# Optimization experiments

Measured on AMD Instinct MI355X. Metric: run time of the kernel, lower is better.

## Reference

```python
import jax, jax.numpy as jnp
import numpy as np

B, S, D, H = 2, 2048, 1024, 16
HD = D // H  # head_dim = 64
ROPE_BASE = 10000.0


def _rope_tables(seq_len, head_dim, dtype):
    inv_freq = 1.0 / (ROPE_BASE ** (jnp.arange(0, head_dim, 2, dtype=jnp.float32) / head_dim))
    t = jnp.arange(seq_len, dtype=jnp.float32)
    freqs = jnp.outer(t, inv_freq)                      # [S, HD/2]
    emb = jnp.concatenate([freqs, freqs], axis=-1)      # [S, HD]
    return jnp.cos(emb).astype(dtype), jnp.sin(emb).astype(dtype)


def _rotate_half(x):
    x1, x2 = jnp.split(x, 2, axis=-1)
    return jnp.concatenate([-x2, x1], axis=-1)


def setup_inputs() -> dict:
    key = jax.random.key(0)
    k0, k1, k2, k3, k4 = jax.random.split(key, 5)
    std = 0.02
    return {
        "hidden_states": jax.random.normal(k0, (B, S, D), dtype=jnp.float32),
        "attention_mask": jnp.ones((B, S), dtype=jnp.int32),
        "Wq": jax.random.normal(k1, (D, D), dtype=jnp.float32) * std,
        "Wk": jax.random.normal(k2, (D, D), dtype=jnp.float32) * std,
        "Wv": jax.random.normal(k3, (D, D), dtype=jnp.float32) * std,
        "Wo": jax.random.normal(k4, (D, D), dtype=jnp.float32) * std,
    }


def reference(hidden_states, attention_mask, Wq, Wk, Wv, Wo):
    b, s, d = hidden_states.shape
    scale = HD ** -0.5

    # torch Linear (no bias): y = x @ W.T, then split heads -> [b, h, s, hd]
    def proj_heads(W):
        y = jnp.einsum('bsd,ed->bse', hidden_states, W)
        return y.reshape(b, s, H, HD).transpose(0, 2, 1, 3)

    q, k, v = proj_heads(Wq), proj_heads(Wk), proj_heads(Wv)

    cos, sin = _rope_tables(s, HD, q.dtype)   # [s, hd]
    cos, sin = cos[None, None], sin[None, None]
    q = q * cos + _rotate_half(q) * sin
    k = k * cos + _rotate_half(k) * sin

    attn = jnp.einsum('bhqd,bhkd->bhqk', q, k) * scale  # [b,h,s,s]
    # mask [b,s] broadcast over heads and query dim (matches expand in torch)
    attn = jnp.where(attention_mask[:, None, None, :] == 0, -jnp.inf, attn)
    attn = jax.nn.softmax(attn, axis=-1)

    out = jnp.einsum('bhqk,bhkd->bhqd', attn, v)
    out = out.transpose(0, 2, 1, 3).reshape(b, s, d)
    return jnp.einsum('bsd,ed->bse', out, Wo)
```

## Files before the change

kernel.cpp:

```cpp
#include <hip/hip_runtime.h>
#include <math.h>

#define B_  2
#define S_  2048
#define D_  1024
#define H_  16
#define HD_ 64
#define M_  (B_*S_)

typedef __attribute__((ext_vector_type(8)))  short s8v;
typedef __attribute__((ext_vector_type(4)))  int   i4v;
typedef __attribute__((ext_vector_type(4)))  float f4v;
typedef __attribute__((ext_vector_type(16))) float f16x;
#define MFMA16(a,b,c) __builtin_amdgcn_mfma_f32_16x16x32_bf16(a,b,c,0,0,0)
#define MFMA32(a,b,c) __builtin_amdgcn_mfma_f32_32x32x16_bf16(a,b,c,0,0,0)

typedef __attribute__((address_space(1))) const unsigned int uint_ga;
typedef __attribute__((address_space(3))) unsigned int       uint_ls;

__device__ __forceinline__ unsigned short f2bf(float x) {
    unsigned u = __float_as_uint(x);
    u += 0x7FFF + ((u >> 16) & 1);
    return (unsigned short)(u >> 16);
}
__device__ __forceinline__ void gld16(const unsigned short* g, short* l) {
    __builtin_amdgcn_global_load_lds((uint_ga*)g, (uint_ls*)l, 16, 0, 0);
}

#define SCALE2 0.1803368801111204f
#define MXF2   16.0f

__global__ __launch_bounds__(256) void cvt_bf16_kernel(
    const float* __restrict__ X,  const float* __restrict__ Wq,
    const float* __restrict__ Wk, const float* __restrict__ Wv,
    const float* __restrict__ Wo,
    unsigned short* __restrict__ Xb,  unsigned short* __restrict__ Wqb,
    unsigned short* __restrict__ Wkb, unsigned short* __restrict__ Wvb,
    unsigned short* __restrict__ Wob, float2* __restrict__ cst)
{
    int y = blockIdx.y;
    if (y == 5) {
        int i = blockIdx.x * 256 + threadIdx.x;
        if (i < S_ * 32) {
            int j = i >> 11, s = i & 2047;
            double inv = pow(10000.0, -(double)j / 32.0);
            double ang = (double)s * inv;
            cst[i] = make_float2((float)cos(ang), (float)sin(ang));
        }
        return;
    }
    const float* src = (y==0)?X:(y==1)?Wq:(y==2)?Wk:(y==3)?Wv:Wo;
    unsigned short* dst = (y==0)?Xb:(y==1)?Wqb:(y==2)?Wkb:(y==3)?Wvb:Wob;
    int n = (y==0) ? (M_*D_) : (D_*D_);
    int i = (blockIdx.x*256 + threadIdx.x)*4;
    if (i >= n) return;
    float4 v = *(const float4*)&src[i];
    ushort4 o;
    o.x = f2bf(v.x); o.y = f2bf(v.y); o.z = f2bf(v.z); o.w = f2bf(v.w);
    *(ushort4*)&dst[i] = o;
}

__device__ __forceinline__ void mfma_128x128(
    const unsigned short* __restrict__ Amat, const unsigned short* __restrict__ Bmat,
    int m0, int n0, short* As, short* Bs, f4v acc[4][4])
{
    int tid = threadIdx.x;
    int l = tid & 63, w = tid >> 6;
    int wm = w >> 1, wn = w & 1;
    int lm = l & 15, qd = l >> 4;
    int lm7 = lm & 7;

    f4v z = {0.f, 0.f, 0.f, 0.f};
#pragma unroll
    for (int mt = 0; mt < 4; mt++)
#pragma unroll
        for (int nt = 0; nt < 4; nt++) acc[mt][nt] = z;

    int rl = l >> 3;
    int kc = (l & 7) ^ rl;
    const unsigned short* aG = Amat + (size_t)(m0 + w*32 + rl) * D_ + kc*8;
    const unsigned short* bG = Bmat + (size_t)(n0 + w*32 + rl) * D_ + kc*8;
    short* aL = As + (w*32)*64;
    short* bL = Bs + (w*32)*64;

#pragma unroll 1
    for (int k0 = 0; k0 < D_; k0 += 64) {
        __syncthreads();
#pragma unroll
        for (int j = 0; j < 4; j++) {
            gld16(aG + k0 + (size_t)j*8*D_, aL + j*8*64);
            gld16(bG + k0 + (size_t)j*8*D_, bL + j*8*64);
        }
        __syncthreads();
#pragma unroll
        for (int half = 0; half < 2; half++) {
            int pc = (half*4 + qd) ^ lm7;
            s8v afr[4], bfr[4];
#pragma unroll
            for (int x = 0; x < 4; x++) {
                afr[x] = *(const s8v*)(As + ((wm*64 + x*16 + lm)*8 + pc)*8);
                bfr[x] = *(const s8v*)(Bs + ((wn*64 + x*16 + lm)*8 + pc)*8);
            }
#pragma unroll
            for (int mt = 0; mt < 4; mt++)
#pragma unroll
                for (int nt = 0; nt < 4; nt++)
                    acc[mt][nt] = MFMA16(afr[mt], bfr[nt], acc[mt][nt]);
        }
    }
}

__global__ __launch_bounds__(256, 2) void qkv_mfma_kernel(
    const unsigned short* __restrict__ Xb,
    const unsigned short* __restrict__ Wqb, const unsigned short* __restrict__ Wkb,
    const unsigned short* __restrict__ Wvb, const float2* __restrict__ cst,
    unsigned short* __restrict__ Q, unsigned short* __restrict__ K,
    unsigned short* __restrict__ Vt)
{
    __shared__ __align__(16) short As[8192], Bs[8192];
    int bx = blockIdx.x, by = blockIdx.y;
    int proj = by >> 3, f8 = by & 7;
    int l = threadIdx.x & 63, w = threadIdx.x >> 6;
    int wm = w >> 1, wn = w & 1, lm = l & 15, qd = l >> 4;

    f4v acc[4][4];
    if (proj < 2) {
        const unsigned short* Wm = proj ? Wkb : Wqb;
        mfma_128x128(Wm, Xb, f8*128, bx*128, As, Bs, acc);

        int b  = (bx*128) >> 11;
        int sb = ((bx*128) & 2047) + wn*64;
        int bh = b*H_ + f8*2 + wm;
        unsigned short* dst = proj ? K : Q;
        float post = proj ? 1.0f : SCALE2;
#pragma unroll
        for (int mt = 0; mt < 4; mt++) {
            float sgn = (mt < 2) ? -1.f : 1.f;
#pragma unroll
            for (int nt = 0; nt < 4; nt++) {
                int s = sb + nt*16 + lm;
                unsigned short ov[4];
#pragma unroll
                for (int r = 0; r < 4; r++) {
                    int d = mt*16 + qd*4 + r;
                    float2 cs = cst[(d & 31)*S_ + s];
                    float v = acc[mt][nt][r];
                    float p = acc[mt^2][nt][r];
                    ov[r] = f2bf((v*cs.x + sgn*p*cs.y) * post);
                }
                ushort4 ou; ou.x=ov[0]; ou.y=ov[1]; ou.z=ov[2]; ou.w=ov[3];
                *(ushort4*)&dst[((size_t)bh*S_ + s)*HD_ + mt*16 + qd*4] = ou;
            }
        }
    } else {
        mfma_128x128(Xb, Wvb, bx*128, f8*128, As, Bs, acc);

        int b  = (bx*128) >> 11;
        int sb = ((bx*128) & 2047) + wm*64;
        int bh = b*H_ + f8*2 + wn;
#pragma unroll
        for (int mt = 0; mt < 4; mt++)
#pragma unroll
            for (int nt = 0; nt < 4; nt++) {
                int dim = nt*16 + lm;
                int s   = sb + mt*16 + qd*4;
                ushort4 ou;
                ou.x = f2bf(acc[mt][nt][0]);
                ou.y = f2bf(acc[mt][nt][1]);
                ou.z = f2bf(acc[mt][nt][2]);
                ou.w = f2bf(acc[mt][nt][3]);
                *(ushort4*)&Vt[((size_t)bh*HD_ + dim)*S_ + s] = ou;
            }
    }
}

__global__ __launch_bounds__(256, 2) void flash_mfma_kernel(
    const unsigned short* __restrict__ Q, const unsigned short* __restrict__ K,
    const unsigned short* __restrict__ Vt, const int* __restrict__ mask,
    unsigned short* __restrict__ AO)
{
    __shared__ __align__(16) short Ksh[2][4096];
    __shared__ __align__(16) short Vsh[2][4096];
    __shared__ __align__(16) float msk[S_];

    int bh = blockIdx.y;
    int b = bh >> 4, h = bh & 15;
    int tid = threadIdx.x;
    int l = tid & 63, w = tid >> 6;
    int lq = l & 31, hf = l >> 5;
    int q0 = blockIdx.x * 128 + w * 32;

    {
        int i0 = tid * 8;
        const int* mp = mask + b * S_ + i0;
#pragma unroll
        for (int jj = 0; jj < 8; jj++)
            msk[i0 + jj] = mp[jj] ? -MXF2 : -3.0e38f;
    }

    const unsigned short* Qr = Q + ((size_t)bh * S_ + q0 + lq) * HD_ + hf * 8;
    s8v qf[4];
#pragma unroll
    for (int dc = 0; dc < 4; dc++) qf[dc] = *(const s8v*)(Qr + dc * 16);

    f16x zz = {0.f};
    f16x oacc[2]; oacc[0] = zz; oacc[1] = zz;
    f16x lacc = zz;
    s8v ones;
#pragma unroll
    for (int j = 0; j < 8; j++) ones[j] = (short)0x3F80;

    const unsigned short* Kb = K  + (size_t)bh * S_ * HD_;
    const unsigned short* Vb = Vt + (size_t)bh * HD_ * S_;

    int fb0 = 2*w, fb1 = 2*w + 1;
    const unsigned short* kS0 = Kb + (size_t)((fb0>>2)*32 + lq) * HD_ + (fb0&3)*16 + hf*8;
    const unsigned short* kS1 = Kb + (size_t)((fb1>>2)*32 + lq) * HD_ + (fb1&3)*16 + hf*8;
    const unsigned short* vS0 = Vb + (size_t)((fb0>>2)*32 + lq) * S_  + (fb0&3)*16 + hf*8;
    const unsigned short* vS1 = Vb + (size_t)((fb1>>2)*32 + lq) * S_  + (fb1&3)*16 + hf*8;

    s8v kr0 = *(const s8v*)(kS0);
    s8v kr1 = *(const s8v*)(kS1);
    s8v vr0 = *(const s8v*)(vS0);
    s8v vr1 = *(const s8v*)(vS1);

#pragma unroll 1
    for (int t = 0; t < S_ / 64; t++) {
        int buf = t & 1;
        *(s8v*)(&Ksh[buf][fb0*512 + l*8]) = kr0;
        *(s8v*)(&Ksh[buf][fb1*512 + l*8]) = kr1;
        *(s8v*)(&Vsh[buf][fb0*512 + l*8]) = vr0;
        *(s8v*)(&Vsh[buf][fb1*512 + l*8]) = vr1;
        __syncthreads();
        if (t < S_/64 - 1) {
            int koff = (t + 1) * 64;
            kr0 = *(const s8v*)(kS0 + (size_t)koff * HD_);
            kr1 = *(const s8v*)(kS1 + (size_t)koff * HD_);
            vr0 = *(const s8v*)(vS0 + koff);
            vr1 = *(const s8v*)(vS1 + koff);
        }

        int mb = t * 64;
        f16x sa0, sa1;
#pragma unroll
        for (int g = 0; g < 4; g++) {
            f4v m0 = *(const f4v*)&msk[mb + g*8 + hf*4];
            f4v m1 = *(const f4v*)&msk[mb + 32 + g*8 + hf*4];
#pragma unroll
            for (int i = 0; i < 4; i++) { sa0[g*4+i] = m0[i]; sa1[g*4+i] = m1[i]; }
        }
#pragma unroll
        for (int dc = 0; dc < 4; dc++) {
            s8v kf0 = *(const s8v*)(&Ksh[buf][(0*4+dc)*512 + l*8]);
            sa0 = MFMA32(kf0, qf[dc], sa0);
        }
#pragma unroll
        for (int dc = 0; dc < 4; dc++) {
            s8v kf1 = *(const s8v*)(&Ksh[buf][(1*4+dc)*512 + l*8]);
            sa1 = MFMA32(kf1, qf[dc], sa1);
        }

        float p[32];
#pragma unroll
        for (int r = 0; r < 16; r++) p[r]      = exp2f(sa0[r]);
#pragma unroll
        for (int r = 0; r < 16; r++) p[16 + r] = exp2f(sa1[r]);

        int pk[16];
#pragma unroll
        for (int m = 0; m < 16; m++)
            pk[m] = __builtin_amdgcn_perm(__float_as_uint(p[2*m+1]),
                                          __float_as_uint(p[2*m]), 0x07060302);

#pragma unroll
        for (int kcc = 0; kcc < 4; kcc++) {
            int a = 4*kcc;
            int x01 = hf ? pk[a]   : pk[a+2];
            int x23 = hf ? pk[a+1] : pk[a+3];
            int y01 = __shfl_xor(x01, 32);
            int y23 = __shfl_xor(x23, 32);
            i4v fr;
            fr.x = hf ? y01 : pk[a];
            fr.y = hf ? y23 : pk[a+1];
            fr.z = hf ? pk[a+2] : y01;
            fr.w = hf ? pk[a+3] : y23;
            s8v pf = __builtin_bit_cast(s8v, fr);
#pragma unroll
            for (int dt = 0; dt < 2; dt++) {
                s8v vf = *(const s8v*)(&Vsh[buf][(dt*4+kcc)*512 + l*8]);
                oacc[dt] = MFMA32(vf, pf, oacc[dt]);
            }
            lacc = MFMA32(ones, pf, lacc);
        }
    }

    float invl = 1.0f / lacc[0];
    int qtok = q0 + lq;
    unsigned short* Or = AO + ((size_t)(b * S_ + qtok)) * D_ + h * HD_;
#pragma unroll
    for (int dt = 0; dt < 2; dt++)
#pragma unroll
        for (int g = 0; g < 4; g++) {
            int d0 = dt*32 + g*8 + hf*4;
            ushort4 o;
            o.x = f2bf(oacc[dt][g*4 + 0] * invl);
            o.y = f2bf(oacc[dt][g*4 + 1] * invl);
            o.z = f2bf(oacc[dt][g*4 + 2] * invl);
            o.w = f2bf(oacc[dt][g*4 + 3] * invl);
            *(ushort4*)&Or[d0] = o;
        }
}

__global__ __launch_bounds__(256, 2) void outproj_mfma_kernel(
    const unsigned short* __restrict__ AO, const unsigned short* __restrict__ Wob,
    float* __restrict__ out)
{
    __shared__ __align__(16) short As[8192], Bs[8192];
    int bx = blockIdx.x, by = blockIdx.y;
    int l = threadIdx.x & 63, w = threadIdx.x >> 6;
    int wm = w >> 1, wn = w & 1, lm = l & 15, qd = l >> 4;

    f4v acc[4][4];
    mfma_128x128(Wob, AO, by*128, bx*128, As, Bs, acc);

#pragma unroll
    for (int mt = 0; mt < 4; mt++)
#pragma unroll
        for (int nt = 0; nt < 4; nt++) {
            int tok = bx*128 + wn*64 + nt*16 + lm;
            int e   = by*128 + wm*64 + mt*16 + qd*4;
            *(f4v*)&out[(size_t)tok*D_ + e] = acc[mt][nt];
        }
}

extern "C" void kernel_launch(void* const* d_in, const int* in_sizes, int n_in,
                              void* d_out, int out_size, void* d_ws, size_t ws_size,
                              hipStream_t stream)
{
    const float* X    = (const float*)d_in[0];
    const int*   mask = (const int*)  d_in[1];
    const float* Wq   = (const float*)d_in[2];
    const float* Wk   = (const float*)d_in[3];
    const float* Wv   = (const float*)d_in[4];
    const float* Wo   = (const float*)d_in[5];
    float* out = (float*)d_out;

    unsigned short* ws = (unsigned short*)d_ws;
    unsigned short* Xb  = ws;
    unsigned short* Wqb = Xb  + (size_t)M_ * D_;
    unsigned short* Wkb = Wqb + (size_t)D_ * D_;
    unsigned short* Wvb = Wkb + (size_t)D_ * D_;
    unsigned short* Wob = Wvb + (size_t)D_ * D_;
    unsigned short* Qb  = Wob + (size_t)D_ * D_;
    unsigned short* Kb  = Qb  + (size_t)M_ * D_;
    unsigned short* Vtb = Kb  + (size_t)M_ * D_;
    unsigned short* AOb = Vtb + (size_t)M_ * D_;
    float2* cst = (float2*)(AOb + (size_t)M_ * D_);

    cvt_bf16_kernel<<<dim3(4096, 6), 256, 0, stream>>>(
        X, Wq, Wk, Wv, Wo, Xb, Wqb, Wkb, Wvb, Wob, cst);
    qkv_mfma_kernel<<<dim3(32, 24), 256, 0, stream>>>(
        Xb, Wqb, Wkb, Wvb, cst, Qb, Kb, Vtb);
    flash_mfma_kernel<<<dim3(S_ / 128, B_ * H_), 256, 0, stream>>>(
        Qb, Kb, Vtb, mask, AOb);
    outproj_mfma_kernel<<<dim3(32, 8), 256, 0, stream>>>(AOb, Wob, out);
}
```

Before: 201.1 us.

## Split flash attention over two key halves and merge partials in a combine kernel

The flash kernel now launches with a third grid dimension of two, so each block handles half of the key sequence and writes unnormalized fp32 partial outputs plus row sums to workspace. A new combine kernel adds the two partials, normalizes, and writes bf16 attention output for the output projection. The aim is to double the number of blocks (and raise the launch-bound occupancy hint) to fill more compute units. The cost is an extra kernel launch and fp32 partial-output traffic, and the workspace is reorganized so the partial buffers overlap regions that are no longer needed. The split relies on a fixed softmax offset (no running max), so the two partials can be summed directly.

```diff
diff --git a/kernel.cpp b/kernel.cpp
--- a/kernel.cpp
+++ b/kernel.cpp
@@ -174,16 +174,17 @@
     }
 }
 
-__global__ __launch_bounds__(256, 2) void flash_mfma_kernel(
+__global__ __launch_bounds__(256, 4) void flash_mfma_kernel(
     const unsigned short* __restrict__ Q, const unsigned short* __restrict__ K,
     const unsigned short* __restrict__ Vt, const int* __restrict__ mask,
-    unsigned short* __restrict__ AO)
+    float* __restrict__ PO0, float* __restrict__ PO1, float* __restrict__ PartL)
 {
     __shared__ __align__(16) short Ksh[2][4096];
     __shared__ __align__(16) short Vsh[2][4096];
-    __shared__ __align__(16) float msk[S_];
+    __shared__ __align__(16) float msk[1024];
 
     int bh = blockIdx.y;
+    int z  = blockIdx.z;
     int b = bh >> 4, h = bh & 15;
     int tid = threadIdx.x;
     int l = tid & 63, w = tid >> 6;
@@ -191,10 +192,10 @@
     int q0 = blockIdx.x * 128 + w * 32;
 
     {
-        int i0 = tid * 8;
-        const int* mp = mask + b * S_ + i0;
-#pragma unroll
-        for (int jj = 0; jj < 8; jj++)
+        int i0 = tid * 4;
+        const int* mp = mask + b * S_ + z * 1024 + i0;
+#pragma unroll
+        for (int jj = 0; jj < 4; jj++)
             msk[i0 + jj] = mp[jj] ? -MXF2 : -3.0e38f;
     }
 
@@ -210,8 +211,8 @@
 #pragma unroll
     for (int j = 0; j < 8; j++) ones[j] = (short)0x3F80;
 
-    const unsigned short* Kb = K  + (size_t)bh * S_ * HD_;
-    const unsigned short* Vb = Vt + (size_t)bh * HD_ * S_;
+    const unsigned short* Kb = K  + (size_t)bh * S_ * HD_ + (size_t)z * 1024 * HD_;
+    const unsigned short* Vb = Vt + (size_t)bh * HD_ * S_ + z * 1024;
 
     int fb0 = 2*w, fb1 = 2*w + 1;
     const unsigned short* kS0 = Kb + (size_t)((fb0>>2)*32 + lq) * HD_ + (fb0&3)*16 + hf*8;
@@ -225,14 +226,14 @@
     s8v vr1 = *(const s8v*)(vS1);
 
 #pragma unroll 1
-    for (int t = 0; t < S_ / 64; t++) {
+    for (int t = 0; t < 16; t++) {
         int buf = t & 1;
         *(s8v*)(&Ksh[buf][fb0*512 + l*8]) = kr0;
         *(s8v*)(&Ksh[buf][fb1*512 + l*8]) = kr1;
         *(s8v*)(&Vsh[buf][fb0*512 + l*8]) = vr0;
         *(s8v*)(&Vsh[buf][fb1*512 + l*8]) = vr1;
         __syncthreads();
-        if (t < S_/64 - 1) {
+        if (t < 15) {
             int koff = (t + 1) * 64;
             kr0 = *(const s8v*)(kS0 + (size_t)koff * HD_);
             kr1 = *(const s8v*)(kS1 + (size_t)koff * HD_);
@@ -294,21 +295,46 @@
         }
     }
 
-    float invl = 1.0f / lacc[0];
+    float* PO = z ? PO1 : PO0;
     int qtok = q0 + lq;
-    unsigned short* Or = AO + ((size_t)(b * S_ + qtok)) * D_ + h * HD_;
+    float* Po = PO + ((size_t)(b * S_ + qtok)) * D_ + h * HD_;
 #pragma unroll
     for (int dt = 0; dt < 2; dt++)
 #pragma unroll
         for (int g = 0; g < 4; g++) {
             int d0 = dt*32 + g*8 + hf*4;
-            ushort4 o;
-            o.x = f2bf(oacc[dt][g*4 + 0] * invl);
-            o.y = f2bf(oacc[dt][g*4 + 1] * invl);
-            o.z = f2bf(oacc[dt][g*4 + 2] * invl);
-            o.w = f2bf(oacc[dt][g*4 + 3] * invl);
-            *(ushort4*)&Or[d0] = o;
-        }
+            f4v v = { oacc[dt][g*4+0], oacc[dt][g*4+1],
+                      oacc[dt][g*4+2], oacc[dt][g*4+3] };
+            *(f4v*)&Po[d0] = v;
+        }
+    if (l < 32)
+        PartL[z * 65536 + bh * S_ + qtok] = lacc[0];
+}
+
+__global__ __launch_bounds__(256) void combine_kernel(
+    const float* __restrict__ P0, const float* __restrict__ P1,
+    const float* __restrict__ PL, unsigned short* __restrict__ AO)
+{
+    int idx = blockIdx.x * 256 + threadIdx.x;
+    int tok = idx >> 6;
+    int seg = (idx & 63) << 4;
+    int bh  = ((tok >> 11) << 4) + (seg >> 6);
+    int q   = tok & 2047;
+    float l0 = PL[bh * S_ + q];
+    float l1 = PL[65536 + bh * S_ + q];
+    float inv = 1.0f / (l0 + l1);
+    size_t base = (size_t)tok * D_ + seg;
+#pragma unroll
+    for (int j = 0; j < 4; j++) {
+        f4v a = *(const f4v*)&P0[base + j*4];
+        f4v c = *(const f4v*)&P1[base + j*4];
+        ushort4 o;
+        o.x = f2bf((a[0] + c[0]) * inv);
+        o.y = f2bf((a[1] + c[1]) * inv);
+        o.z = f2bf((a[2] + c[2]) * inv);
+        o.w = f2bf((a[3] + c[3]) * inv);
+        *(ushort4*)&AO[base + j*4] = o;
+    }
 }
 
 __global__ __launch_bounds__(256, 2) void outproj_mfma_kernel(
@@ -345,23 +371,29 @@
     const float* Wo   = (const float*)d_in[5];
     float* out = (float*)d_out;
 
+    const size_t MU = 1024 * 1024;
     unsigned short* ws = (unsigned short*)d_ws;
     unsigned short* Xb  = ws;
-    unsigned short* Wqb = Xb  + (size_t)M_ * D_;
-    unsigned short* Wkb = Wqb + (size_t)D_ * D_;
-    unsigned short* Wvb = Wkb + (size_t)D_ * D_;
-    unsigned short* Wob = Wvb + (size_t)D_ * D_;
-    unsigned short* Qb  = Wob + (size_t)D_ * D_;
-    unsigned short* Kb  = Qb  + (size_t)M_ * D_;
-    unsigned short* Vtb = Kb  + (size_t)M_ * D_;
-    unsigned short* AOb = Vtb + (size_t)M_ * D_;
-    float2* cst = (float2*)(AOb + (size_t)M_ * D_);
+    unsigned short* Wqb = ws + 4*MU;
+    unsigned short* Wkb = ws + 5*MU;
+    unsigned short* Wvb = ws + 6*MU;
+    unsigned short* Wob = ws + 8*MU;
+    unsigned short* Qb  = ws + 9*MU;
+    unsigned short* Kb  = ws + 13*MU;
+    unsigned short* Vtb = ws + 17*MU;
+    unsigned short* AOb = ws + 21*MU;
+    float2* cst = (float2*)(ws + 25*MU);
+
+    float* PartO0 = (float*)ws;
+    float* PartO1 = (float*)(ws + 25*MU + 512*1024);
+    float* PartL  = PartO1 + (size_t)M_ * D_;
 
     cvt_bf16_kernel<<<dim3(4096, 6), 256, 0, stream>>>(
         X, Wq, Wk, Wv, Wo, Xb, Wqb, Wkb, Wvb, Wob, cst);
     qkv_mfma_kernel<<<dim3(32, 24), 256, 0, stream>>>(
         Xb, Wqb, Wkb, Wvb, cst, Qb, Kb, Vtb);
-    flash_mfma_kernel<<<dim3(S_ / 128, B_ * H_), 256, 0, stream>>>(
-        Qb, Kb, Vtb, mask, AOb);
+    flash_mfma_kernel<<<dim3(S_ / 128, B_ * H_, 2), 256, 0, stream>>>(
+        Qb, Kb, Vtb, mask, PartO0, PartO1, PartL);
+    combine_kernel<<<1024, 256, 0, stream>>>(PartO0, PartO1, PartL, AOb);
     outproj_mfma_kernel<<<dim3(32, 8), 256, 0, stream>>>(AOb, Wob, out);
 }
```

Result: slower. 242.8 us (+20.7%).
